# Kernel tuning notes

Measured on AMD Instinct MI355X. Metric: run time of the kernel, lower is better.

## Reference

```python
import jax, jax.numpy as jnp
import numpy as np

# ---- constants from init_kwargs ----
CUTOFF = 6.0
BOX = np.array([50.0, 50.0, 50.0], dtype=np.float32)  # orthorhombic box lengths
MAX_NUM_NEIGHBORS = 32
ADD_SELF_LOOPS = True
N_ATOMS = 8192


def setup_inputs() -> dict:
    key = jax.random.key(0)
    k1, _ = jax.random.split(key)
    # positions uniform inside the periodic box
    pos = jax.random.uniform(k1, (N_ATOMS, 3), dtype=jnp.float32) * jnp.asarray(BOX)
    batch = jnp.zeros((N_ATOMS,), dtype=jnp.int64)  # single system
    return {"pos": pos, "batch": batch}


def _build_neighbors(pos, batch):
    """Periodic radius-graph via minimum-image convention, fixed K per node.

    Equivalent to tiling periodic images within cutoff + radius_graph with
    max_num_neighbors, but expressed with fixed shapes: each node keeps its
    K nearest in-cutoff neighbors (self included when ADD_SELF_LOOPS),
    padded with self-loops.
    """
    N = pos.shape[0]
    box = jnp.asarray(BOX, pos.dtype)
    diff = pos[:, None, :] - pos[None, :, :]              # [N, N, 3]
    diff = diff - jnp.round(diff / box) * box             # minimum image
    d2 = jnp.sum(diff * diff, axis=-1)                    # [N, N]
    valid = (batch[:, None] == batch[None, :]) & (d2 <= CUTOFF * CUTOFF)
    if not ADD_SELF_LOOPS:
        valid = valid & ~jnp.eye(N, dtype=bool)
    masked = jnp.where(valid, d2, jnp.inf)
    neg_vals, idx = jax.lax.top_k(-masked, MAX_NUM_NEIGHBORS)  # K smallest d2
    has_nbr = jnp.isfinite(neg_vals)                       # [N, K]
    rows = jnp.arange(N, dtype=idx.dtype)[:, None]
    src = jnp.broadcast_to(rows, idx.shape).ravel()        # [N*K]
    dst = jnp.where(has_nbr, idx, rows).ravel()            # pad -> self-loop
    return src, dst


def reference(pos, batch):
    src, dst = _build_neighbors(pos, batch)
    edge_index = jnp.stack([src, dst])                     # [2, N*K]
    # NOTE: faithful to the torch module: edge_vec uses raw (unwrapped)
    # positions after mapping periodic-image indices back to originals.
    edge_vec = pos[src] - pos[dst]                         # [N*K, 3]
    mask = src != dst
    v2 = jnp.sum(edge_vec * edge_vec, axis=-1)
    safe = jnp.where(mask, v2, 1.0)                        # avoid sqrt(0) grad
    edge_weight = jnp.where(mask, jnp.sqrt(safe), 0.0)     # self-loops -> 0
    return edge_index, edge_weight, edge_vec
```

## Files before the change

kernel.cpp:

```cpp
#include <hip/hip_runtime.h>
#include <stdint.h>


constexpr int NATOMS = 8192;
constexpr int KNB    = 32;
constexpr int CAP    = 128;
constexpr int NK     = NATOMS * KNB;

__global__ __launch_bounds__(256) void radius_graph_1pass(
    const float* __restrict__ pos,
    float* __restrict__ out)
{
#pragma clang fp contract(off)
    __shared__ unsigned long long s_key[4][CAP];
    __shared__ int s_cnt[4];

    const int wv   = threadIdx.x >> 6;
    const int lane = threadIdx.x & 63;
    const int i    = (blockIdx.x << 2) + wv;

    const float xi = pos[3*i + 0];
    const float yi = pos[3*i + 1];
    const float zi = pos[3*i + 2];

    if (lane == 0) s_cnt[wv] = 0;
    __syncthreads();

    for (int j = lane; j < NATOMS; j += 64) {
        float dx = xi - pos[3*j + 0];
        float dy = yi - pos[3*j + 1];
        float dz = zi - pos[3*j + 2];
        dx = (dx >  25.0f) ? dx - 50.0f : dx;
        dx = (dx < -25.0f) ? dx + 50.0f : dx;
        dy = (dy >  25.0f) ? dy - 50.0f : dy;
        dy = (dy < -25.0f) ? dy + 50.0f : dy;
        dz = (dz >  25.0f) ? dz - 50.0f : dz;
        dz = (dz < -25.0f) ? dz + 50.0f : dz;
        float sx = dx * dx;
        float sy = dy * dy;
        float sz = dz * dz;
        float d2 = sx + sz;
        d2 = d2 + sy;
        if (d2 <= 36.0f) {
            unsigned long long key =
                ((((unsigned long long)__float_as_uint(d2)) << 13)
                 | (unsigned long long)(unsigned)j) + 1ULL;
            int slot = atomicAdd(&s_cnt[wv], 1);
            if (slot < CAP) s_key[wv][slot] = key;
        }
    }
    __syncthreads();

    int M = s_cnt[wv];
    if (M > CAP) M = CAP;

    unsigned long long k0 = ~0ULL, k1 = ~0ULL;
    if (lane < M)      k0 = s_key[wv][lane];
    if (lane + 64 < M) k1 = s_key[wv][lane + 64];

    unsigned long long prev = 0ULL;
    int mydst = i;
    for (int k = 0; k < KNB; ++k) {
        unsigned long long best = ~0ULL;
        if (k0 > prev && k0 < best) best = k0;
        if (k1 > prev && k1 < best) best = k1;
        #pragma unroll
        for (int off = 32; off > 0; off >>= 1) {
            unsigned long long o = __shfl_xor(best, off, 64);
            if (o < best) best = o;
        }
        int dst = (best == ~0ULL) ? i : (int)((best - 1ULL) & 0x1fffULL);
        if (lane == k) mydst = dst;
        prev = best;
    }

    if (lane < KNB) {
        const int e = i * KNB + lane;
        const int j = mydst;
        float ex = xi - pos[3*j + 0];
        float ey = yi - pos[3*j + 1];
        float ez = zi - pos[3*j + 2];
        float v2 = ex * ex;
        v2 = v2 + ey * ey;
        v2 = v2 + ez * ez;
        float w = (j != i) ? sqrtf(v2) : 0.0f;

        out[e]                = (float)i;
        out[NK + e]           = (float)j;
        out[2 * NK + e]       = w;
        out[3 * NK + 3*e + 0] = ex;
        out[3 * NK + 3*e + 1] = ey;
        out[3 * NK + 3*e + 2] = ez;
    }
}

extern "C" void kernel_launch(void* const* d_in, const int* in_sizes, int n_in,
                              void* d_out, int out_size, void* d_ws, size_t ws_size,
                              hipStream_t stream) {
    const float* pos = (const float*)d_in[0];
    float* out = (float*)d_out;
    radius_graph_1pass<<<NATOMS / 4, 256, 0, stream>>>(pos, out);
}
```

Before: 143.1 us.

## Replace all-pairs neighbor scan with 8x8x8 cell-list search

Adds a memset and a cell-binning kernel that sorts atoms into an 8x8x8 periodic grid (cell width 6.25, at least the cutoff). The main kernel then scans only the 27 neighboring cells instead of all 8192 atoms, which removes most of the O(N^2) distance work. The all-pairs kernel is kept as a fallback when the workspace is too small. In exchange it adds two extra launches and global atomics, and it silently drops atoms if a cell holds more than 96.

```diff
diff --git a/kernel.cpp b/kernel.cpp
--- a/kernel.cpp
+++ b/kernel.cpp
@@ -2,13 +2,34 @@
 #include <stdint.h>
 
 
-constexpr int NATOMS = 8192;
-constexpr int KNB    = 32;
-constexpr int CAP    = 128;
-constexpr int NK     = NATOMS * KNB;
-
-__global__ __launch_bounds__(256) void radius_graph_1pass(
+constexpr int NATOMS  = 8192;
+constexpr int KNB     = 32;
+constexpr int CAP     = 128;
+constexpr int NK      = NATOMS * KNB;
+constexpr int CELLCAP = 96;
+constexpr size_t WS_NEEDED = (512 + 512 * (size_t)CELLCAP) * sizeof(int);
+
+__device__ __forceinline__ int cell_of(float x) {
+    int c = (int)(x * 0.16f);
+    return c > 7 ? 7 : (c < 0 ? 0 : c);
+}
+
+__global__ __launch_bounds__(256) void build_cells(
+    const float* __restrict__ pos, int* __restrict__ cnt, int* __restrict__ list)
+{
+    int i = blockIdx.x * 256 + threadIdx.x;
+    if (i >= NATOMS) return;
+    int cx = cell_of(pos[3*i + 0]);
+    int cy = cell_of(pos[3*i + 1]);
+    int cz = cell_of(pos[3*i + 2]);
+    int c  = (cz * 8 + cy) * 8 + cx;
+    int slot = atomicAdd(&cnt[c], 1);
+    if (slot < CELLCAP) list[c * CELLCAP + slot] = i;
+}
+
+__global__ __launch_bounds__(256) void radius_graph_cells(
     const float* __restrict__ pos,
+    const int* __restrict__ cnt, const int* __restrict__ list,
     float* __restrict__ out)
 {
 #pragma clang fp contract(off)
@@ -26,27 +47,38 @@
     if (lane == 0) s_cnt[wv] = 0;
     __syncthreads();
 
-    for (int j = lane; j < NATOMS; j += 64) {
-        float dx = xi - pos[3*j + 0];
-        float dy = yi - pos[3*j + 1];
-        float dz = zi - pos[3*j + 2];
-        dx = (dx >  25.0f) ? dx - 50.0f : dx;
-        dx = (dx < -25.0f) ? dx + 50.0f : dx;
-        dy = (dy >  25.0f) ? dy - 50.0f : dy;
-        dy = (dy < -25.0f) ? dy + 50.0f : dy;
-        dz = (dz >  25.0f) ? dz - 50.0f : dz;
-        dz = (dz < -25.0f) ? dz + 50.0f : dz;
-        float sx = dx * dx;
-        float sy = dy * dy;
-        float sz = dz * dz;
-        float d2 = sx + sz;
-        d2 = d2 + sy;
-        if (d2 <= 36.0f) {
-            unsigned long long key =
-                ((((unsigned long long)__float_as_uint(d2)) << 13)
-                 | (unsigned long long)(unsigned)j) + 1ULL;
-            int slot = atomicAdd(&s_cnt[wv], 1);
-            if (slot < CAP) s_key[wv][slot] = key;
+    const int cx = cell_of(xi), cy = cell_of(yi), cz = cell_of(zi);
+
+    for (int oz = -1; oz <= 1; ++oz)
+    for (int oy = -1; oy <= 1; ++oy)
+    for (int ox = -1; ox <= 1; ++ox) {
+        const int c = (((cz + oz) & 7) * 8 + ((cy + oy) & 7)) * 8 + ((cx + ox) & 7);
+        int n = cnt[c];
+        n = n > CELLCAP ? CELLCAP : n;
+        const int* cl = list + c * CELLCAP;
+        for (int t = lane; t < n; t += 64) {
+            const int j = cl[t];
+            float dx = xi - pos[3*j + 0];
+            float dy = yi - pos[3*j + 1];
+            float dz = zi - pos[3*j + 2];
+            dx = (dx >  25.0f) ? dx - 50.0f : dx;
+            dx = (dx < -25.0f) ? dx + 50.0f : dx;
+            dy = (dy >  25.0f) ? dy - 50.0f : dy;
+            dy = (dy < -25.0f) ? dy + 50.0f : dy;
+            dz = (dz >  25.0f) ? dz - 50.0f : dz;
+            dz = (dz < -25.0f) ? dz + 50.0f : dz;
+            float sx = dx * dx;
+            float sy = dy * dy;
+            float sz = dz * dz;
+            float d2 = sx + sz;
+            d2 = d2 + sy;
+            if (d2 <= 36.0f) {
+                unsigned long long key =
+                    ((((unsigned long long)__float_as_uint(d2)) << 13)
+                     | (unsigned long long)(unsigned)j) + 1ULL;
+                int slot = atomicAdd(&s_cnt[wv], 1);
+                if (slot < CAP) s_key[wv][slot] = key;
+            }
         }
     }
     __syncthreads();
@@ -94,10 +126,78 @@
     }
 }
 
+__global__ __launch_bounds__(256) void radius_graph_1pass(
+    const float* __restrict__ pos, float* __restrict__ out)
+{
+#pragma clang fp contract(off)
+    __shared__ unsigned long long s_key[4][CAP];
+    __shared__ int s_cnt[4];
+    const int wv = threadIdx.x >> 6, lane = threadIdx.x & 63;
+    const int i  = (blockIdx.x << 2) + wv;
+    const float xi = pos[3*i+0], yi = pos[3*i+1], zi = pos[3*i+2];
+    if (lane == 0) s_cnt[wv] = 0;
+    __syncthreads();
+    for (int j = lane; j < NATOMS; j += 64) {
+        float dx = xi - pos[3*j+0], dy = yi - pos[3*j+1], dz = zi - pos[3*j+2];
+        dx = (dx >  25.0f) ? dx - 50.0f : dx;
+        dx = (dx < -25.0f) ? dx + 50.0f : dx;
+        dy = (dy >  25.0f) ? dy - 50.0f : dy;
+        dy = (dy < -25.0f) ? dy + 50.0f : dy;
+        dz = (dz >  25.0f) ? dz - 50.0f : dz;
+        dz = (dz < -25.0f) ? dz + 50.0f : dz;
+        float sx = dx*dx, sy = dy*dy, sz = dz*dz;
+        float d2 = sx + sz; d2 = d2 + sy;
+        if (d2 <= 36.0f) {
+            unsigned long long key =
+                ((((unsigned long long)__float_as_uint(d2)) << 13)
+                 | (unsigned long long)(unsigned)j) + 1ULL;
+            int slot = atomicAdd(&s_cnt[wv], 1);
+            if (slot < CAP) s_key[wv][slot] = key;
+        }
+    }
+    __syncthreads();
+    int M = s_cnt[wv]; if (M > CAP) M = CAP;
+    unsigned long long k0 = ~0ULL, k1 = ~0ULL;
+    if (lane < M)      k0 = s_key[wv][lane];
+    if (lane + 64 < M) k1 = s_key[wv][lane + 64];
+    unsigned long long prev = 0ULL;
+    int mydst = i;
+    for (int k = 0; k < KNB; ++k) {
+        unsigned long long best = ~0ULL;
+        if (k0 > prev && k0 < best) best = k0;
+        if (k1 > prev && k1 < best) best = k1;
+        #pragma unroll
+        for (int off = 32; off > 0; off >>= 1) {
+            unsigned long long o = __shfl_xor(best, off, 64);
+            if (o < best) best = o;
+        }
+        int dst = (best == ~0ULL) ? i : (int)((best - 1ULL) & 0x1fffULL);
+        if (lane == k) mydst = dst;
+        prev = best;
+    }
+    if (lane < KNB) {
+        const int e = i * KNB + lane;
+        const int j = mydst;
+        float ex = xi - pos[3*j+0], ey = yi - pos[3*j+1], ez = zi - pos[3*j+2];
+        float v2 = ex*ex; v2 = v2 + ey*ey; v2 = v2 + ez*ez;
+        float w = (j != i) ? sqrtf(v2) : 0.0f;
+        out[e] = (float)i;  out[NK + e] = (float)j;  out[2*NK + e] = w;
+        out[3*NK + 3*e+0] = ex; out[3*NK + 3*e+1] = ey; out[3*NK + 3*e+2] = ez;
+    }
+}
+
 extern "C" void kernel_launch(void* const* d_in, const int* in_sizes, int n_in,
                               void* d_out, int out_size, void* d_ws, size_t ws_size,
                               hipStream_t stream) {
     const float* pos = (const float*)d_in[0];
     float* out = (float*)d_out;
-    radius_graph_1pass<<<NATOMS / 4, 256, 0, stream>>>(pos, out);
-}
+    if (ws_size >= WS_NEEDED) {
+        int* cnt  = (int*)d_ws;
+        int* list = cnt + 512;
+        hipMemsetAsync(cnt, 0, 512 * sizeof(int), stream);
+        build_cells<<<NATOMS / 256, 256, 0, stream>>>(pos, cnt, list);
+        radius_graph_cells<<<NATOMS / 4, 256, 0, stream>>>(pos, cnt, list, out);
+    } else {
+        radius_graph_1pass<<<NATOMS / 4, 256, 0, stream>>>(pos, out);
+    }
+}
```

Measured after the change: 121.1 us. 1.18x faster.
